# Performance work log

Measured on AMD Instinct MI355X. Metric: run time of the kernel, lower is better.

Reference implementation:

```python
import jax, jax.numpy as jnp
import numpy as np

N_DEPTH = 4
N_STACKS = 2
INPUT_SIZE = 1024
HIDDEN_SIZE = 4096
HU = HIDDEN_SIZE // (N_DEPTH * N_STACKS)  # unit_hidden_size = 512
BATCH = 4096


def setup_inputs() -> dict:
    key = jax.random.key(0)
    ks = jax.random.split(key, 8)
    inp = {
        "input": jax.random.normal(ks[0], (BATCH, INPUT_SIZE), dtype=jnp.float32),
        "state": jax.random.normal(ks[1], (2, N_STACKS, BATCH, HIDDEN_SIZE), dtype=jnp.float32),
        # LSTMCell params; residualStack=True -> every cell input dim = INPUT_SIZE
        "W_ih": jax.random.normal(ks[2], (N_DEPTH, N_STACKS, 4 * HU, INPUT_SIZE), dtype=jnp.float32) * 0.05,
        "W_hh": jax.random.normal(ks[3], (N_DEPTH, N_STACKS, 4 * HU, HU), dtype=jnp.float32) * 0.05,
        "b_ih": jax.random.normal(ks[4], (N_DEPTH, N_STACKS, 4 * HU), dtype=jnp.float32) * 0.05,
        "b_hh": jax.random.normal(ks[5], (N_DEPTH, N_STACKS, 4 * HU), dtype=jnp.float32) * 0.05,
        # stacks_proj: Linear(HU, INPUT_SIZE)
        "proj_W": jax.random.normal(ks[6], (INPUT_SIZE, HU), dtype=jnp.float32) * 0.05,
        "proj_b": jax.random.normal(ks[7], (INPUT_SIZE,), dtype=jnp.float32) * 0.05,
    }
    return inp


def _lstm_cell(x, hx, cx, w_ih, w_hh, b_ih, b_hh):
    # gates: [B, 4*HU], PyTorch LSTMCell gate order: i, f, g, o
    gates = x @ w_ih.T + b_ih + hx @ w_hh.T + b_hh
    i_g, f_g, g_g, o_g = jnp.split(gates, 4, axis=-1)
    i_g = jax.nn.sigmoid(i_g)
    f_g = jax.nn.sigmoid(f_g)
    g_g = jnp.tanh(g_g)
    o_g = jax.nn.sigmoid(o_g)
    c_out = f_g * cx + i_g * g_g
    h_out = o_g * jnp.tanh(c_out)
    return h_out, c_out


def reference(input, state, W_ih, W_hh, b_ih, b_hh, proj_W, proj_b):
    # residual=True, residualStack=True
    h_depth, c_depth = [], []
    for i in range(N_DEPTH):
        s, e = i * HU, (i + 1) * HU
        hs, cs = [], []
        dec_input = input
        h_out = None
        for j in range(N_STACKS):
            if j > 0:
                # residualStack: dec_input = dec_input + stacks_proj(h_out)
                dec_input = dec_input + h_out @ proj_W.T + proj_b
            hx = state[0, j, :, s:e]
            cx = state[1, j, :, s:e]
            h_out, c_out = _lstm_cell(dec_input, hx, cx,
                                      W_ih[i, j], W_hh[i, j], b_ih[i, j], b_hh[i, j])
            hs.append(h_out + hx)  # residual=True
            cs.append(c_out)
        h_depth.append(jnp.stack(hs, 0))  # [nStacks, B, HU]
        c_depth.append(jnp.stack(cs, 0))
    # hidden dim is laid out by depth slice: newState[..., i*HU:(i+1)*HU]
    newH = jnp.concatenate(h_depth, axis=-1)  # [nStacks, B, hidden_size]
    newC = jnp.concatenate(c_depth, axis=-1)
    newState = jnp.stack([newH, newC], axis=0)  # [2, nStacks, B, hidden_size]
    ho = newState[0, -1]  # [B, hidden_size]
    return ho, newState
```

## Files before the change

kernel.cpp:

```cpp
#include <hip/hip_runtime.h>
#include <cstdint>
#include <cstddef>

#define B_   4096
#define ISZ  1024
#define SW   4096
#define OHW  2048
#define HU_  512
#define NG   2048

typedef float f32x4 __attribute__((ext_vector_type(4)));
typedef short bf16x8 __attribute__((ext_vector_type(8)));

__device__ __forceinline__ short f2bf(float x) {
    union { float f; unsigned u; } v; v.f = x;
    unsigned r = v.u + 0x7fffu + ((v.u >> 16) & 1u);
    return (short)(r >> 16);
}
__device__ __forceinline__ float sigm(float x)   { return 1.f / (1.f + __expf(-x)); }
__device__ __forceinline__ float tanh_f(float x) { return 2.f / (1.f + __expf(-2.f * x)) - 1.f; }

__device__ __forceinline__ void async16(const void* g, void* l) {
    __builtin_amdgcn_global_load_lds((__attribute__((address_space(1))) void*)g,
                                     (__attribute__((address_space(3))) void*)l,
                                     16, 0, 0);
}

__global__ __launch_bounds__(256) void cvt_kernel(const float* __restrict__ src,
                                                  short* __restrict__ dst, long n) {
    long i = ((long)blockIdx.x * 256 + threadIdx.x) * 8;
    if (i >= n) return;
    float4 a = *(const float4*)(src + i);
    float4 b = *(const float4*)(src + i + 4);
    bf16x8 o;
    o[0] = f2bf(a.x); o[1] = f2bf(a.y); o[2] = f2bf(a.z); o[3] = f2bf(a.w);
    o[4] = f2bf(b.x); o[5] = f2bf(b.y); o[6] = f2bf(b.z); o[7] = f2bf(b.w);
    *(bf16x8*)(dst + i) = o;
}

__global__ __launch_bounds__(256) void cvt_h_kernel(const float* __restrict__ src,
                                                    short* __restrict__ dst) {
    long i = ((long)blockIdx.x * 256 + threadIdx.x) * 8;
    long row = i >> 11;
    long c   = i & 2047;
    const float* s = src + row * SW + c;
    float4 a = *(const float4*)(s);
    float4 b = *(const float4*)(s + 4);
    bf16x8 o;
    o[0] = f2bf(a.x); o[1] = f2bf(a.y); o[2] = f2bf(a.z); o[3] = f2bf(a.w);
    o[4] = f2bf(b.x); o[5] = f2bf(b.y); o[6] = f2bf(b.z); o[7] = f2bf(b.w);
    *(bf16x8*)(dst + i) = o;
}

__global__ __launch_bounds__(256) void gates_kernel(
    const short* __restrict__ A1, long a1_dstride,
    const short* __restrict__ Hb,
    const short* __restrict__ Wihb, const short* __restrict__ Whhb,
    const float* __restrict__ b_ih, const float* __restrict__ b_hh,
    const float* __restrict__ state,
    float* __restrict__ out_ho, float* __restrict__ out_state,
    short* __restrict__ h0b,
    int j)
{
    __shared__ __align__(16) short sA[128 * 64];
    __shared__ __align__(16) short sB[128 * 64];

    const int t    = threadIdx.x;
    const int wave = t >> 6, lane = t & 63;
    const int ln16 = lane & 15, q = lane >> 4;
    const int d  = blockIdx.z;
    const int M0 = blockIdx.x * 128;
    const int h0 = blockIdx.y * 32;
    const int s  = d * HU_;

    const short* A1d = A1 + (size_t)d * a1_dstride;
    const short* A2  = Hb + (size_t)j * B_ * OHW + s;
    const short* W1  = Wihb + (size_t)(d * 2 + j) * NG * ISZ;
    const short* W2  = Whhb + (size_t)(d * 2 + j) * NG * HU_;
    const float* bi_ = b_ih + (size_t)(d * 2 + j) * NG;
    const float* bh_ = b_hh + (size_t)(d * 2 + j) * NG;

    const int srow = wave * 8 + (lane >> 3);
    const int scol = (((lane & 7) ^ (lane >> 3)) << 3);

    f32x4 acc[2][8];
#pragma unroll
    for (int mt = 0; mt < 2; mt++)
#pragma unroll
        for (int nt = 0; nt < 8; nt++) acc[mt][nt] = (f32x4){0.f, 0.f, 0.f, 0.f};

    auto compute_tile = [&]() {
#pragma unroll
        for (int ks = 0; ks < 2; ks++) {
            const int kb = ks * 4 + q;
            bf16x8 a[2], b[8];
#pragma unroll
            for (int mt = 0; mt < 2; mt++) {
                const int m = wave * 32 + mt * 16 + ln16;
                a[mt] = *(const bf16x8*)&sA[m * 64 + ((kb ^ (m & 7)) << 3)];
            }
#pragma unroll
            for (int nt = 0; nt < 8; nt++) {
                const int n = nt * 16 + ln16;
                b[nt] = *(const bf16x8*)&sB[n * 64 + ((kb ^ (n & 7)) << 3)];
            }
#pragma unroll
            for (int mt = 0; mt < 2; mt++)
#pragma unroll
                for (int nt = 0; nt < 8; nt++)
                    acc[mt][nt] = __builtin_amdgcn_mfma_f32_16x16x32_bf16(a[mt], b[nt], acc[mt][nt], 0, 0, 0);
        }
    };

    for (int k0 = 0; k0 < ISZ; k0 += 64) {
#pragma unroll
        for (int it = 0; it < 4; it++)
            async16(A1d + (size_t)(M0 + it * 32 + srow) * ISZ + k0 + scol,
                    &sA[(it * 32 + wave * 8) * 64]);
#pragma unroll
        for (int it = 0; it < 4; it++)
            async16(W1 + (size_t)(it * HU_ + h0 + srow) * ISZ + k0 + scol,
                    &sB[(it * 32 + wave * 8) * 64]);
        __syncthreads();
        compute_tile();
        __syncthreads();
    }
    for (int k0 = 0; k0 < HU_; k0 += 64) {
#pragma unroll
        for (int it = 0; it < 4; it++)
            async16(A2 + (size_t)(M0 + it * 32 + srow) * OHW + k0 + scol,
                    &sA[(it * 32 + wave * 8) * 64]);
#pragma unroll
        for (int it = 0; it < 4; it++)
            async16(W2 + (size_t)(it * HU_ + h0 + srow) * HU_ + k0 + scol,
                    &sB[(it * 32 + wave * 8) * 64]);
        __syncthreads();
        compute_tile();
        __syncthreads();
    }

#pragma unroll
    for (int mt = 0; mt < 2; mt++) {
#pragma unroll
        for (int nh = 0; nh < 2; nh++) {
            const int h   = h0 + nh * 16 + ln16;
            const int col = s + h;
            const float b_i = bi_[h]          + bh_[h];
            const float b_f = bi_[512 + h]    + bh_[512 + h];
            const float b_g = bi_[1024 + h]   + bh_[1024 + h];
            const float b_o = bi_[1536 + h]   + bh_[1536 + h];
            const f32x4 ai = acc[mt][0 + nh];
            const f32x4 af = acc[mt][2 + nh];
            const f32x4 ag = acc[mt][4 + nh];
            const f32x4 ao = acc[mt][6 + nh];
#pragma unroll
            for (int r = 0; r < 4; r++) {
                const int m = M0 + wave * 32 + mt * 16 + q * 4 + r;
                const float hx = state[((size_t)(j)     * B_ + m) * SW + col];
                const float cx = state[((size_t)(2 + j) * B_ + m) * SW + col];
                const float gi = sigm(ai[r] + b_i);
                const float gf = sigm(af[r] + b_f);
                const float gg = tanh_f(ag[r] + b_g);
                const float go = sigm(ao[r] + b_o);
                const float c_out = gf * cx + gi * gg;
                const float h_out = go * tanh_f(c_out);
                out_state[((size_t)(j)     * B_ + m) * OHW + col] = h_out + hx;
                out_state[((size_t)(2 + j) * B_ + m) * OHW + col] = c_out;
                if (j == 1) out_ho[(size_t)m * OHW + col] = h_out + hx;
                else        h0b[((size_t)d * B_ + m) * HU_ + h] = f2bf(h_out);
            }
        }
    }
}

__global__ __launch_bounds__(256) void proj_kernel(
    const short* __restrict__ h0b, const short* __restrict__ PWb,
    const float* __restrict__ input, const float* __restrict__ proj_b,
    short* __restrict__ dec1b)
{
    __shared__ __align__(16) short sA[128 * 64];
    __shared__ __align__(16) short sB[128 * 64];

    const int t    = threadIdx.x;
    const int wave = t >> 6, lane = t & 63;
    const int ln16 = lane & 15, q = lane >> 4;
    const int d  = blockIdx.z;
    const int M0 = blockIdx.x * 128;
    const int N0 = blockIdx.y * 128;

    const short* A = h0b + (size_t)d * B_ * HU_;

    const int srow = wave * 8 + (lane >> 3);
    const int scol = (((lane & 7) ^ (lane >> 3)) << 3);

    f32x4 acc[2][8];
#pragma unroll
    for (int mt = 0; mt < 2; mt++)
#pragma unroll
        for (int nt = 0; nt < 8; nt++) acc[mt][nt] = (f32x4){0.f, 0.f, 0.f, 0.f};

    for (int k0 = 0; k0 < HU_; k0 += 64) {
#pragma unroll
        for (int it = 0; it < 4; it++)
            async16(A + (size_t)(M0 + it * 32 + srow) * HU_ + k0 + scol,
                    &sA[(it * 32 + wave * 8) * 64]);
#pragma unroll
        for (int it = 0; it < 4; it++)
            async16(PWb + (size_t)(N0 + it * 32 + srow) * HU_ + k0 + scol,
                    &sB[(it * 32 + wave * 8) * 64]);
        __syncthreads();
#pragma unroll
        for (int ks = 0; ks < 2; ks++) {
            const int kb = ks * 4 + q;
            bf16x8 a[2], b[8];
#pragma unroll
            for (int mt = 0; mt < 2; mt++) {
                const int m = wave * 32 + mt * 16 + ln16;
                a[mt] = *(const bf16x8*)&sA[m * 64 + ((kb ^ (m & 7)) << 3)];
            }
#pragma unroll
            for (int nt = 0; nt < 8; nt++) {
                const int n = nt * 16 + ln16;
                b[nt] = *(const bf16x8*)&sB[n * 64 + ((kb ^ (n & 7)) << 3)];
            }
#pragma unroll
            for (int mt = 0; mt < 2; mt++)
#pragma unroll
                for (int nt = 0; nt < 8; nt++)
                    acc[mt][nt] = __builtin_amdgcn_mfma_f32_16x16x32_bf16(a[mt], b[nt], acc[mt][nt], 0, 0, 0);
        }
        __syncthreads();
    }

#pragma unroll
    for (int mt = 0; mt < 2; mt++) {
#pragma unroll
        for (int nt = 0; nt < 8; nt++) {
            const int n = N0 + nt * 16 + ln16;
            const float pb = proj_b[n];
#pragma unroll
            for (int r = 0; r < 4; r++) {
                const int m = M0 + wave * 32 + mt * 16 + q * 4 + r;
                const float y = acc[mt][nt][r] + input[(size_t)m * ISZ + n] + pb;
                dec1b[((size_t)d * B_ + m) * ISZ + n] = f2bf(y);
            }
        }
    }
}

extern "C" void kernel_launch(void* const* d_in, const int* in_sizes, int n_in,
                              void* d_out, int out_size, void* d_ws, size_t ws_size,
                              hipStream_t stream)
{
    const float* input  = (const float*)d_in[0];
    const float* state  = (const float*)d_in[1];
    const float* W_ih   = (const float*)d_in[2];
    const float* W_hh   = (const float*)d_in[3];
    const float* b_ih   = (const float*)d_in[4];
    const float* b_hh   = (const float*)d_in[5];
    const float* proj_W = (const float*)d_in[6];
    const float* proj_b = (const float*)d_in[7];

    float* out_ho    = (float*)d_out;
    float* out_state = out_ho + (size_t)B_ * OHW;

    short* ws    = (short*)d_ws;
    short* Wihb  = ws;
    short* Whhb  = Wihb + (size_t)8 * NG * ISZ;
    short* PWb   = Whhb + (size_t)8 * NG * HU_;
    short* Hb    = PWb  + (size_t)ISZ * HU_;
    short* h0b   = Hb   + (size_t)2 * B_ * OHW;
    short* dec1b = h0b  + (size_t)4 * B_ * HU_;
    short* Xb    = dec1b;

    {
        long n;
        n = (long)8 * NG * ISZ;  cvt_kernel<<<dim3((unsigned)(n / 8 / 256)), 256, 0, stream>>>(W_ih,   Wihb, n);
        n = (long)8 * NG * HU_;  cvt_kernel<<<dim3((unsigned)(n / 8 / 256)), 256, 0, stream>>>(W_hh,   Whhb, n);
        n = (long)ISZ * HU_;     cvt_kernel<<<dim3((unsigned)(n / 8 / 256)), 256, 0, stream>>>(proj_W, PWb,  n);
        n = (long)B_ * ISZ;      cvt_kernel<<<dim3((unsigned)(n / 8 / 256)), 256, 0, stream>>>(input,  Xb,   n);
        n = (long)2 * B_ * OHW;  cvt_h_kernel<<<dim3((unsigned)(n / 8 / 256)), 256, 0, stream>>>(state, Hb);
    }

    gates_kernel<<<dim3(32, 16, 4), 256, 0, stream>>>(Xb, 0L, Hb, Wihb, Whhb,
                                                      b_ih, b_hh, state,
                                                      out_ho, out_state, h0b, 0);
    proj_kernel<<<dim3(32, 8, 4), 256, 0, stream>>>(h0b, PWb, input, proj_b, dec1b);
    gates_kernel<<<dim3(32, 16, 4), 256, 0, stream>>>(dec1b, (long)B_ * ISZ, Hb, Wihb, Whhb,
                                                      b_ih, b_hh, state,
                                                      out_ho, out_state, nullptr, 1);
}
```

Measured before the change: 838.0 us.

## Rewrite gates GEMM as 256x256 tile with double-buffered LDS pipeline

Replaces the 128x128-tile gates kernel with a 512-thread, 256x256-tile kernel. It double-buffers its LDS in 128KB of dynamic shared memory, interleaves async global-to-LDS loads with MFMA blocks using explicit waitcnt and barrier, raises wave priority around MFMA, and swizzles block ids. The aim is to hide load latency behind compute, raise arithmetic intensity per tile and improve L2 locality. The costs are much higher register and LDS pressure, which may limit occupancy.

```diff
diff --git a/kernel.cpp b/kernel.cpp
--- a/kernel.cpp
+++ b/kernel.cpp
@@ -25,6 +25,8 @@
                                      (__attribute__((address_space(3))) void*)l,
                                      16, 0, 0);
 }
+
+#define PIPE_SYNC(N) asm volatile("s_waitcnt vmcnt(" #N ")\n\ts_barrier" ::: "memory")
 
 __global__ __launch_bounds__(256) void cvt_kernel(const float* __restrict__ src,
                                                   short* __restrict__ dst, long n) {
@@ -52,7 +54,26 @@
     *(bf16x8*)(dst + i) = o;
 }
 
-__global__ __launch_bounds__(256) void gates_kernel(
+#define MMA_BLK(BB, AR0, N0)                                                      \
+  do {                                                                            \
+    __builtin_amdgcn_s_setprio(1);                                                \
+    _Pragma("unroll")                                                             \
+    for (int mtl = 0; mtl < 4; ++mtl) {                                           \
+      _Pragma("unroll")                                                           \
+      for (int nn = 0; nn < 2; ++nn) {                                            \
+        _Pragma("unroll")                                                         \
+        for (int ks = 0; ks < 2; ++ks) {                                          \
+          acc[(AR0) + mtl][(N0) + nn] = __builtin_amdgcn_mfma_f32_16x16x32_bf16(  \
+              aR[mtl][ks], BB[nn][ks], acc[(AR0) + mtl][(N0) + nn], 0, 0, 0);     \
+        }                                                                         \
+      }                                                                           \
+    }                                                                             \
+    __builtin_amdgcn_s_setprio(0);                                                \
+  } while (0)
+
+#define GROW(rb) (((((rb) >> 4) & 3) << 9) + h0 + ((((rb) >> 6)) << 4) + ((rb) & 15))
+
+__global__ __launch_bounds__(512, 2) void gates2_kernel(
     const short* __restrict__ A1, long a1_dstride,
     const short* __restrict__ Hb,
     const short* __restrict__ Wihb, const short* __restrict__ Whhb,
@@ -62,16 +83,22 @@
     short* __restrict__ h0b,
     int j)
 {
-    __shared__ __align__(16) short sA[128 * 64];
-    __shared__ __align__(16) short sB[128 * 64];
-
-    const int t    = threadIdx.x;
-    const int wave = t >> 6, lane = t & 63;
-    const int ln16 = lane & 15, q = lane >> 4;
-    const int d  = blockIdx.z;
-    const int M0 = blockIdx.x * 128;
-    const int h0 = blockIdx.y * 32;
-    const int s  = d * HU_;
+    extern __shared__ short lds[];
+
+    const int tid  = threadIdx.x;
+    const int wave = tid >> 6;
+    const int lane = tid & 63;
+    const int wm   = wave >> 2;
+    const int wn   = wave & 3;
+    const int ln16 = lane & 15;
+    const int q    = (lane >> 4) & 3;
+
+    const int id  = blockIdx.x;
+    const int swz = (id & 7) * 64 + (id >> 3);
+    const int M0  = (swz & 15) * 256;
+    const int h0  = ((swz >> 4) & 7) * 64;
+    const int d   = swz >> 7;
+    const int s   = d * HU_;
 
     const short* A1d = A1 + (size_t)d * a1_dstride;
     const short* A2  = Hb + (size_t)j * B_ * OHW + s;
@@ -80,95 +107,126 @@
     const float* bi_ = b_ih + (size_t)(d * 2 + j) * NG;
     const float* bh_ = b_hh + (size_t)(d * 2 + j) * NG;
 
-    const int srow = wave * 8 + (lane >> 3);
-    const int scol = (((lane & 7) ^ (lane >> 3)) << 3);
-
-    f32x4 acc[2][8];
-#pragma unroll
-    for (int mt = 0; mt < 2; mt++)
-#pragma unroll
-        for (int nt = 0; nt < 8; nt++) acc[mt][nt] = (f32x4){0.f, 0.f, 0.f, 0.f};
-
-    auto compute_tile = [&]() {
-#pragma unroll
-        for (int ks = 0; ks < 2; ks++) {
-            const int kb = ks * 4 + q;
-            bf16x8 a[2], b[8];
-#pragma unroll
-            for (int mt = 0; mt < 2; mt++) {
-                const int m = wave * 32 + mt * 16 + ln16;
-                a[mt] = *(const bf16x8*)&sA[m * 64 + ((kb ^ (m & 7)) << 3)];
-            }
-#pragma unroll
-            for (int nt = 0; nt < 8; nt++) {
-                const int n = nt * 16 + ln16;
-                b[nt] = *(const bf16x8*)&sB[n * 64 + ((kb ^ (n & 7)) << 3)];
-            }
-#pragma unroll
-            for (int mt = 0; mt < 2; mt++)
-#pragma unroll
-                for (int nt = 0; nt < 8; nt++)
-                    acc[mt][nt] = __builtin_amdgcn_mfma_f32_16x16x32_bf16(a[mt], b[nt], acc[mt][nt], 0, 0, 0);
-        }
-    };
-
-    for (int k0 = 0; k0 < ISZ; k0 += 64) {
-#pragma unroll
-        for (int it = 0; it < 4; it++)
-            async16(A1d + (size_t)(M0 + it * 32 + srow) * ISZ + k0 + scol,
-                    &sA[(it * 32 + wave * 8) * 64]);
-#pragma unroll
-        for (int it = 0; it < 4; it++)
-            async16(W1 + (size_t)(it * HU_ + h0 + srow) * ISZ + k0 + scol,
-                    &sB[(it * 32 + wave * 8) * 64]);
-        __syncthreads();
-        compute_tile();
-        __syncthreads();
-    }
-    for (int k0 = 0; k0 < HU_; k0 += 64) {
-#pragma unroll
-        for (int it = 0; it < 4; it++)
-            async16(A2 + (size_t)(M0 + it * 32 + srow) * OHW + k0 + scol,
-                    &sA[(it * 32 + wave * 8) * 64]);
-#pragma unroll
-        for (int it = 0; it < 4; it++)
-            async16(W2 + (size_t)(it * HU_ + h0 + srow) * HU_ + k0 + scol,
-                    &sB[(it * 32 + wave * 8) * 64]);
-        __syncthreads();
-        compute_tile();
-        __syncthreads();
-    }
-
-#pragma unroll
-    for (int mt = 0; mt < 2; mt++) {
-#pragma unroll
-        for (int nh = 0; nh < 2; nh++) {
-            const int h   = h0 + nh * 16 + ln16;
-            const int col = s + h;
-            const float b_i = bi_[h]          + bh_[h];
-            const float b_f = bi_[512 + h]    + bh_[512 + h];
-            const float b_g = bi_[1024 + h]   + bh_[1024 + h];
-            const float b_o = bi_[1536 + h]   + bh_[1536 + h];
-            const f32x4 ai = acc[mt][0 + nh];
-            const f32x4 af = acc[mt][2 + nh];
-            const f32x4 ag = acc[mt][4 + nh];
-            const f32x4 ao = acc[mt][6 + nh];
-#pragma unroll
-            for (int r = 0; r < 4; r++) {
-                const int m = M0 + wave * 32 + mt * 16 + q * 4 + r;
-                const float hx = state[((size_t)(j)     * B_ + m) * SW + col];
-                const float cx = state[((size_t)(2 + j) * B_ + m) * SW + col];
-                const float gi = sigm(ai[r] + b_i);
-                const float gf = sigm(af[r] + b_f);
-                const float gg = tanh_f(ag[r] + b_g);
-                const float go = sigm(ao[r] + b_o);
-                const float c_out = gf * cx + gi * gg;
-                const float h_out = go * tanh_f(c_out);
-                out_state[((size_t)(j)     * B_ + m) * OHW + col] = h_out + hx;
-                out_state[((size_t)(2 + j) * B_ + m) * OHW + col] = c_out;
-                if (j == 1) out_ho[(size_t)m * OHW + col] = h_out + hx;
-                else        h0b[((size_t)d * B_ + m) * HU_ + h] = f2bf(h_out);
-            }
+    const int srow = tid >> 3;
+    const int scol = (((tid & 7) ^ ((tid >> 3) & 7)) << 3);
+
+    const short* As = A1d;
+    const short* Bs = W1;
+    unsigned aoff0 = (unsigned)((M0 +   0 + srow) * ISZ + scol);
+    unsigned aoff1 = (unsigned)((M0 +  64 + srow) * ISZ + scol);
+    unsigned aoff2 = (unsigned)((M0 + 128 + srow) * ISZ + scol);
+    unsigned aoff3 = (unsigned)((M0 + 192 + srow) * ISZ + scol);
+    unsigned boff0 = (unsigned)(GROW(      srow) * ISZ + scol);
+    unsigned boff1 = (unsigned)(GROW( 64 + srow) * ISZ + scol);
+    unsigned boff2 = (unsigned)(GROW(128 + srow) * ISZ + scol);
+    unsigned boff3 = (unsigned)(GROW(192 + srow) * ISZ + scol);
+
+    const int swz0 = ((q    ) ^ (ln16 & 7)) << 4;
+    const int swz1 = ((q + 4) ^ (ln16 & 7)) << 4;
+    const char* ldsb = (const char*)lds;
+
+    f32x4 acc[8][4];
+#pragma unroll
+    for (int i = 0; i < 8; ++i)
+#pragma unroll
+        for (int n = 0; n < 4; ++n) acc[i][n] = (f32x4){0.f, 0.f, 0.f, 0.f};
+
+    bf16x8 aR[4][2];
+    bf16x8 b01[2][2];
+    bf16x8 b23[2][2];
+
+    auto stA = [&](unsigned off, int it, int nbuf, int kofs) {
+        async16(As + off + kofs, lds + nbuf * 32768 + (it * 64 + wave * 8) * 64);
+    };
+    auto stB = [&](unsigned off, int it, int nbuf, int kofs) {
+        async16(Bs + off + kofs, lds + nbuf * 32768 + 16384 + (it * 64 + wave * 8) * 64);
+    };
+    auto rdA = [&](int buf, int hi) {
+#pragma unroll
+        for (int mtl = 0; mtl < 4; ++mtl) {
+            const int row = wm * 128 + hi * 64 + mtl * 16 + ln16;
+            aR[mtl][0] = *(const bf16x8*)(ldsb + buf * 65536 + row * 128 + swz0);
+            aR[mtl][1] = *(const bf16x8*)(ldsb + buf * 65536 + row * 128 + swz1);
+        }
+    };
+    auto rdB = [&](bf16x8 (&bb)[2][2], int buf, int nt0) {
+#pragma unroll
+        for (int nn = 0; nn < 2; ++nn) {
+            const int row = wn * 64 + (nt0 + nn) * 16 + ln16;
+            bb[nn][0] = *(const bf16x8*)(ldsb + buf * 65536 + 32768 + row * 128 + swz0);
+            bb[nn][1] = *(const bf16x8*)(ldsb + buf * 65536 + 32768 + row * 128 + swz1);
+        }
+    };
+
+    stB(boff0, 0, 0, 0); stB(boff1, 1, 0, 0); stB(boff2, 2, 0, 0); stB(boff3, 3, 0, 0);
+    stA(aoff0, 0, 0, 0); stA(aoff2, 2, 0, 0); stA(aoff1, 1, 0, 0); stA(aoff3, 3, 0, 0);
+    PIPE_SYNC(0);
+
+    auto do_tile = [&](int t, int kofs) {
+        const int buf = t & 1, nbuf = buf ^ 1;
+        stB(boff0, 0, nbuf, kofs); stB(boff1, 1, nbuf, kofs);
+        rdA(buf, 0); rdB(b01, buf, 0);
+        MMA_BLK(b01, 0, 0);
+        stB(boff2, 2, nbuf, kofs); stB(boff3, 3, nbuf, kofs);
+        rdB(b23, buf, 2);
+        MMA_BLK(b23, 0, 2);
+        PIPE_SYNC(4);
+        stA(aoff0, 0, nbuf, kofs); stA(aoff2, 2, nbuf, kofs);
+        rdA(buf, 1);
+        MMA_BLK(b23, 4, 2);
+        stA(aoff1, 1, nbuf, kofs); stA(aoff3, 3, nbuf, kofs);
+        MMA_BLK(b01, 4, 0);
+        PIPE_SYNC(2);
+    };
+
+    for (int t = 0; t < 15; ++t) do_tile(t, (t + 1) * 64);
+
+    As = A2; Bs = W2;
+    aoff0 = (unsigned)((M0 +   0 + srow) * OHW + scol);
+    aoff1 = (unsigned)((M0 +  64 + srow) * OHW + scol);
+    aoff2 = (unsigned)((M0 + 128 + srow) * OHW + scol);
+    aoff3 = (unsigned)((M0 + 192 + srow) * OHW + scol);
+    boff0 = (unsigned)(GROW(      srow) * HU_ + scol);
+    boff1 = (unsigned)(GROW( 64 + srow) * HU_ + scol);
+    boff2 = (unsigned)(GROW(128 + srow) * HU_ + scol);
+    boff3 = (unsigned)(GROW(192 + srow) * HU_ + scol);
+
+    for (int t = 15; t < 23; ++t) do_tile(t, (t - 15) * 64);
+
+    {
+        rdA(1, 0); rdB(b01, 1, 0);
+        MMA_BLK(b01, 0, 0);
+        rdB(b23, 1, 2);
+        MMA_BLK(b23, 0, 2);
+        PIPE_SYNC(0);
+        rdA(1, 1);
+        MMA_BLK(b23, 4, 2);
+        MMA_BLK(b01, 4, 0);
+    }
+
+    const int h   = h0 + wn * 16 + ln16;
+    const int col = s + h;
+    const float b_i = bi_[h]          + bh_[h];
+    const float b_f = bi_[512 + h]    + bh_[512 + h];
+    const float b_g = bi_[1024 + h]   + bh_[1024 + h];
+    const float b_o = bi_[1536 + h]   + bh_[1536 + h];
+#pragma unroll
+    for (int mt = 0; mt < 8; ++mt) {
+#pragma unroll
+        for (int r = 0; r < 4; ++r) {
+            const int m = M0 + wm * 128 + mt * 16 + q * 4 + r;
+            const float hx = state[((size_t)(j)     * B_ + m) * SW + col];
+            const float cx = state[((size_t)(2 + j) * B_ + m) * SW + col];
+            const float gi = sigm(acc[mt][0][r] + b_i);
+            const float gf = sigm(acc[mt][1][r] + b_f);
+            const float gg = tanh_f(acc[mt][2][r] + b_g);
+            const float go = sigm(acc[mt][3][r] + b_o);
+            const float c_out = gf * cx + gi * gg;
+            const float h_out = go * tanh_f(c_out);
+            out_state[((size_t)(j)     * B_ + m) * OHW + col] = h_out + hx;
+            out_state[((size_t)(2 + j) * B_ + m) * OHW + col] = c_out;
+            if (j == 1) out_ho[(size_t)m * OHW + col] = h_out + hx;
+            else        h0b[((size_t)d * B_ + m) * HU_ + h] = f2bf(h_out);
         }
     }
 }
@@ -273,6 +331,13 @@
     short* dec1b = h0b  + (size_t)4 * B_ * HU_;
     short* Xb    = dec1b;
 
+    static bool s_attr = false;
+    if (!s_attr) {
+        (void)hipFuncSetAttribute(reinterpret_cast<const void*>(gates2_kernel),
+                                  hipFuncAttributeMaxDynamicSharedMemorySize, 131072);
+        s_attr = true;
+    }
+
     {
         long n;
         n = (long)8 * NG * ISZ;  cvt_kernel<<<dim3((unsigned)(n / 8 / 256)), 256, 0, stream>>>(W_ih,   Wihb, n);
@@ -282,11 +347,11 @@
         n = (long)2 * B_ * OHW;  cvt_h_kernel<<<dim3((unsigned)(n / 8 / 256)), 256, 0, stream>>>(state, Hb);
     }
 
-    gates_kernel<<<dim3(32, 16, 4), 256, 0, stream>>>(Xb, 0L, Hb, Wihb, Whhb,
-                                                      b_ih, b_hh, state,
-                                                      out_ho, out_state, h0b, 0);
+    gates2_kernel<<<dim3(512), dim3(512), 131072, stream>>>(Xb, 0L, Hb, Wihb, Whhb,
+                                                            b_ih, b_hh, state,
+                                                            out_ho, out_state, h0b, 0);
     proj_kernel<<<dim3(32, 8, 4), 256, 0, stream>>>(h0b, PWb, input, proj_b, dec1b);
-    gates_kernel<<<dim3(32, 16, 4), 256, 0, stream>>>(dec1b, (long)B_ * ISZ, Hb, Wihb, Whhb,
-                                                      b_ih, b_hh, state,
-                                                      out_ho, out_state, nullptr, 1);
-}
+    gates2_kernel<<<dim3(512), dim3(512), 131072, stream>>>(dec1b, (long)B_ * ISZ, Hb, Wihb, Whhb,
+                                                            b_ih, b_hh, state,
+                                                            out_ho, out_state, nullptr, 1);
+}
```

New measurement: 723.0 us. 13.7% less time.
